# Performance work log

Hardware: AMD Instinct MI355X
Metric: run time of the kernel (lower is better)

The kernel has to match this reference:

```python
import jax, jax.numpy as jnp
import numpy as np

T = 16777216            # flat replay-buffer length (timesteps)
DISCOUNT = 0.99         # gamma
FINAL_REWARD = 0.0      # bootstrap value for the last timestep
TERM_PROB = 0.001       # ~1000-step episodes


def setup_inputs() -> dict:
    key = jax.random.key(0)
    k1, k2 = jax.random.split(key)
    reward = jax.random.normal(k1, (T,), dtype=jnp.float32)
    terminal = jax.random.bernoulli(k2, TERM_PROB, (T,))
    return {"terminal": terminal, "reward": reward}


def _discounted_cumret(terminal, reward):
    # Reverse-time linear recurrence (same math as tf.scan over reversed seq):
    #   c_t = r_t                      if terminal_t
    #   c_t = r_t + discount * c_{t+1} otherwise
    # i.e. c_t = a_t * c_{t+1} + b_t with a_t = discount*(1-term_t), b_t = r_t.
    # Expressed as a (log-depth) associative scan over the reversed sequence.
    a = jnp.where(terminal, jnp.zeros((), reward.dtype),
                  jnp.asarray(DISCOUNT, reward.dtype))
    a_rev = a[::-1]
    b_rev = reward[::-1]
    # fold the initializer (final_reward) into the first reversed element
    b_rev = b_rev.at[0].add(a_rev[0] * jnp.asarray(FINAL_REWARD, reward.dtype))

    def combine(e1, e2):
        # composition of affine maps x -> a*x + b (e1 applied first)
        a1, b1 = e1
        a2, b2 = e2
        return a1 * a2, a2 * b1 + b2

    _, y_rev = jax.lax.associative_scan(combine, (a_rev, b_rev))
    return y_rev[::-1]


def reference(terminal, reward):
    return _discounted_cumret(terminal, reward)
```

## Files before the change

kernel.cpp:

```cpp
#include <hip/hip_runtime.h>


constexpr int   TPB  = 256;
constexpr int   IPT  = 4;
constexpr int   TILE = TPB * IPT;
constexpr float DISC = 0.99f;

__device__ __forceinline__ void wave_suffix_scan(float& A, float& B, int lane) {
    #pragma unroll
    for (int off = 1; off < 64; off <<= 1) {
        float oA = __shfl_down(A, off, 64);
        float oB = __shfl_down(B, off, 64);
        if (lane + off < 64) { B = A * oB + B; A = A * oA; }
    }
}

__global__ __launch_bounds__(TPB) void k_agg(const int* __restrict__ term,
                                             const float* __restrict__ rew,
                                             float2* __restrict__ agg,
                                             long long T) {
    __shared__ float2 sW[TPB / 64];
    const int t = threadIdx.x;
    const int lane = t & 63, wav = t >> 6;
    const long long base = (long long)blockIdx.x * TILE + (long long)t * IPT;

    float r[IPT], a[IPT];
    if (base + IPT <= T) {
        float4 rv = *(const float4*)(rew + base);
        int4   tv = *(const int4*)(term + base);
        r[0]=rv.x; r[1]=rv.y; r[2]=rv.z; r[3]=rv.w;
        a[0]=tv.x?0.f:DISC; a[1]=tv.y?0.f:DISC; a[2]=tv.z?0.f:DISC; a[3]=tv.w?0.f:DISC;
    } else {
        #pragma unroll
        for (int k = 0; k < IPT; ++k) {
            long long i = base + k;
            if (i < T) { r[k]=rew[i]; a[k]=term[i]?0.f:DISC; }
            else       { r[k]=0.f;   a[k]=1.f; }
        }
    }

    float A = 1.f, B = 0.f;
    #pragma unroll
    for (int k = IPT - 1; k >= 0; --k) { B = a[k]*B + r[k]; A = a[k]*A; }

    wave_suffix_scan(A, B, lane);
    if (lane == 0) sW[wav] = make_float2(A, B);
    __syncthreads();
    if (t == 0) {
        float2 g = sW[0];
        #pragma unroll
        for (int w = 1; w < TPB / 64; ++w) {
            float2 h = sW[w];
            g.y = g.x * h.y + g.y; g.x = g.x * h.x;
        }
        agg[blockIdx.x] = g;
    }
}

__global__ __launch_bounds__(TPB) void k_mid(const float2* __restrict__ agg,
                                             float* __restrict__ yin,
                                             int numTiles) {
    __shared__ float2 sW[TPB / 64];
    const int t = threadIdx.x;
    const int lane = t & 63, wav = t >> 6;
    const int cpt = (numTiles + TPB - 1) / TPB;
    const int lo = t * cpt;

    float A = 1.f, B = 0.f;
    for (int k = cpt - 1; k >= 0; --k) {
        int g = lo + k;
        if (g < numTiles) {
            float2 v = agg[g];
            B = v.x * B + v.y; A = v.x * A;
        }
    }

    float IA = A, IB = B;
    wave_suffix_scan(IA, IB, lane);
    if (lane == 0) sW[wav] = make_float2(IA, IB);
    __syncthreads();

    float EWA = 1.f, EWB = 0.f;
    #pragma unroll
    for (int w = 0; w < TPB / 64; ++w)
        if (w > wav) { float2 h = sW[w]; EWB = EWA*h.y + EWB; EWA = EWA*h.x; }

    float EA = __shfl_down(IA, 1, 64);
    float EB = __shfl_down(IB, 1, 64);
    if (lane == 63) { EA = 1.f; EB = 0.f; }

    float x1 = EWB;
    float v  = EA * x1 + EB;
    for (int k = cpt - 1; k >= 0; --k) {
        int g = lo + k;
        if (g < numTiles) {
            yin[g] = v;
            float2 q = agg[g];
            v = q.x * v + q.y;
        }
    }
}

__global__ __launch_bounds__(TPB) void k_apply(const int* __restrict__ term,
                                               const float* __restrict__ rew,
                                               const float* __restrict__ yin,
                                               float* __restrict__ out,
                                               long long T) {
    __shared__ float2 sW[TPB / 64];
    const int t = threadIdx.x;
    const int lane = t & 63, wav = t >> 6;
    const long long base = (long long)blockIdx.x * TILE + (long long)t * IPT;

    float r[IPT], a[IPT];
    const bool fast = (base + IPT <= T);
    if (fast) {
        float4 rv = *(const float4*)(rew + base);
        int4   tv = *(const int4*)(term + base);
        r[0]=rv.x; r[1]=rv.y; r[2]=rv.z; r[3]=rv.w;
        a[0]=tv.x?0.f:DISC; a[1]=tv.y?0.f:DISC; a[2]=tv.z?0.f:DISC; a[3]=tv.w?0.f:DISC;
    } else {
        #pragma unroll
        for (int k = 0; k < IPT; ++k) {
            long long i = base + k;
            if (i < T) { r[k]=rew[i]; a[k]=term[i]?0.f:DISC; }
            else       { r[k]=0.f;   a[k]=1.f; }
        }
    }

    float A = 1.f, B = 0.f;
    #pragma unroll
    for (int k = IPT - 1; k >= 0; --k) { B = a[k]*B + r[k]; A = a[k]*A; }

    float IA = A, IB = B;
    wave_suffix_scan(IA, IB, lane);
    if (lane == 0) sW[wav] = make_float2(IA, IB);
    __syncthreads();

    float EWA = 1.f, EWB = 0.f;
    #pragma unroll
    for (int w = 0; w < TPB / 64; ++w)
        if (w > wav) { float2 h = sW[w]; EWB = EWA*h.y + EWB; EWA = EWA*h.x; }

    float EA = __shfl_down(IA, 1, 64);
    float EB = __shfl_down(IB, 1, 64);
    if (lane == 63) { EA = 1.f; EB = 0.f; }

    const float yt = yin[blockIdx.x];
    float x1 = EWA * yt + EWB;
    float y  = EA * x1 + EB;

    float yv[IPT];
    #pragma unroll
    for (int k = IPT - 1; k >= 0; --k) { y = a[k]*y + r[k]; yv[k] = y; }

    if (fast) {
        *(float4*)(out + base) = make_float4(yv[0], yv[1], yv[2], yv[3]);
    } else {
        #pragma unroll
        for (int k = 0; k < IPT; ++k) {
            long long i = base + k;
            if (i < T) out[i] = yv[k];
        }
    }
}

extern "C" void kernel_launch(void* const* d_in, const int* in_sizes, int n_in,
                              void* d_out, int out_size, void* d_ws, size_t ws_size,
                              hipStream_t stream) {
    const int*   term = (const int*)d_in[0];
    const float* rew  = (const float*)d_in[1];
    float*       out  = (float*)d_out;

    const long long T = (long long)in_sizes[1];
    const int numTiles = (int)((T + TILE - 1) / TILE);

    float2* agg = (float2*)d_ws;
    float*  yin = (float*)(agg + numTiles);

    k_agg  <<<numTiles, TPB, 0, stream>>>(term, rew, agg, T);
    k_mid  <<<1,        TPB, 0, stream>>>(agg, yin, numTiles);
    k_apply<<<numTiles, TPB, 0, stream>>>(term, rew, yin, out, T);
}
```

Before: 215.5 us.

## Replace reduce-then-scan with local scan plus sparse carry fix-up

The three-kernel reduce/mid/apply scan becomes two kernels. The first computes each block's local suffix scan and writes the output directly, along with the block aggregate and the index of the last terminal in the block. The second kernel has each block recompute the carry-in from all later block aggregates, then add carry*gamma^d only to the elements after the block's last terminal, so the inputs are read only once. Tiles grow to 32 items per thread, the terminal flags are packed into a bitmask, and the correction uses exp2f, which can differ slightly in rounding from sequential multiplication.

```diff
diff --git a/kernel.cpp b/kernel.cpp
--- a/kernel.cpp
+++ b/kernel.cpp
@@ -2,9 +2,10 @@
 
 
 constexpr int   TPB  = 256;
-constexpr int   IPT  = 4;
+constexpr int   IPT  = 32;
 constexpr int   TILE = TPB * IPT;
 constexpr float DISC = 0.99f;
+constexpr float L2DISC = -0.0144995696f;
 
 __device__ __forceinline__ void wave_suffix_scan(float& A, float& B, int lane) {
     #pragma unroll
@@ -15,152 +16,147 @@
     }
 }
 
-__global__ __launch_bounds__(TPB) void k_agg(const int* __restrict__ term,
-                                             const float* __restrict__ rew,
-                                             float2* __restrict__ agg,
-                                             long long T) {
-    __shared__ float2 sW[TPB / 64];
+__global__ __launch_bounds__(TPB) void k_local(
+        const int* __restrict__ term, const float* __restrict__ rew,
+        float* __restrict__ out, float2* __restrict__ agg,
+        int* __restrict__ lastT, long long T) {
+    __shared__ float2 sWA[TPB / 64];
+    __shared__ int    sLast[TPB / 64];
+
     const int t = threadIdx.x;
     const int lane = t & 63, wav = t >> 6;
-    const long long base = (long long)blockIdx.x * TILE + (long long)t * IPT;
+    const int b = blockIdx.x;
+    const long long lo   = (long long)b * TILE;
+    const long long base = lo + (long long)t * IPT;
+    const bool fast = (base + IPT <= T);
 
-    float r[IPT], a[IPT];
-    if (base + IPT <= T) {
-        float4 rv = *(const float4*)(rew + base);
-        int4   tv = *(const int4*)(term + base);
-        r[0]=rv.x; r[1]=rv.y; r[2]=rv.z; r[3]=rv.w;
-        a[0]=tv.x?0.f:DISC; a[1]=tv.y?0.f:DISC; a[2]=tv.z?0.f:DISC; a[3]=tv.w?0.f:DISC;
+    float r[IPT];
+    unsigned mask = 0;
+    if (fast) {
+        const float4* rp = (const float4*)(rew + base);
+        const int4*   tp = (const int4*)(term + base);
+        #pragma unroll
+        for (int q = 0; q < IPT / 4; ++q) {
+            float4 rv = rp[q];
+            int4   tv = tp[q];
+            r[4*q+0] = rv.x; r[4*q+1] = rv.y; r[4*q+2] = rv.z; r[4*q+3] = rv.w;
+            mask |= (tv.x ? 1u : 0u) << (4*q+0);
+            mask |= (tv.y ? 1u : 0u) << (4*q+1);
+            mask |= (tv.z ? 1u : 0u) << (4*q+2);
+            mask |= (tv.w ? 1u : 0u) << (4*q+3);
+        }
     } else {
         #pragma unroll
         for (int k = 0; k < IPT; ++k) {
             long long i = base + k;
-            if (i < T) { r[k]=rew[i]; a[k]=term[i]?0.f:DISC; }
-            else       { r[k]=0.f;   a[k]=1.f; }
+            if (i < T) { r[k] = rew[i]; mask |= (term[i] ? 1u : 0u) << k; }
+            else       { r[k] = 0.f; }
         }
     }
 
     float A = 1.f, B = 0.f;
     #pragma unroll
-    for (int k = IPT - 1; k >= 0; --k) { B = a[k]*B + r[k]; A = a[k]*A; }
-
-    wave_suffix_scan(A, B, lane);
-    if (lane == 0) sW[wav] = make_float2(A, B);
-    __syncthreads();
-    if (t == 0) {
-        float2 g = sW[0];
-        #pragma unroll
-        for (int w = 1; w < TPB / 64; ++w) {
-            float2 h = sW[w];
-            g.y = g.x * h.y + g.y; g.x = g.x * h.x;
-        }
-        agg[blockIdx.x] = g;
-    }
-}
-
-__global__ __launch_bounds__(TPB) void k_mid(const float2* __restrict__ agg,
-                                             float* __restrict__ yin,
-                                             int numTiles) {
-    __shared__ float2 sW[TPB / 64];
-    const int t = threadIdx.x;
-    const int lane = t & 63, wav = t >> 6;
-    const int cpt = (numTiles + TPB - 1) / TPB;
-    const int lo = t * cpt;
-
-    float A = 1.f, B = 0.f;
-    for (int k = cpt - 1; k >= 0; --k) {
-        int g = lo + k;
-        if (g < numTiles) {
-            float2 v = agg[g];
-            B = v.x * B + v.y; A = v.x * A;
-        }
+    for (int k = IPT - 1; k >= 0; --k) {
+        float ak = ((mask >> k) & 1u) ? 0.f : DISC;
+        if (!fast && base + k >= T) ak = 1.f;
+        B = ak * B + r[k]; A = ak * A;
     }
 
     float IA = A, IB = B;
     wave_suffix_scan(IA, IB, lane);
-    if (lane == 0) sW[wav] = make_float2(IA, IB);
+
+    int myLast = mask ? (int)(base + (31 - __clz(mask))) : -1;
+    #pragma unroll
+    for (int off = 32; off > 0; off >>= 1)
+        myLast = max(myLast, __shfl_down(myLast, off, 64));
+
+    if (lane == 0) { sWA[wav] = make_float2(IA, IB); sLast[wav] = myLast; }
     __syncthreads();
+
+    if (t == 0) {
+        float2 g = sWA[0];
+        int lt = sLast[0];
+        #pragma unroll
+        for (int w = 1; w < TPB / 64; ++w) {
+            float2 h = sWA[w];
+            g.y = g.x * h.y + g.y; g.x = g.x * h.x;
+            lt = max(lt, sLast[w]);
+        }
+        agg[b] = g;
+        lastT[b] = max(lt, (int)lo - 1);
+    }
 
     float EWA = 1.f, EWB = 0.f;
     #pragma unroll
     for (int w = 0; w < TPB / 64; ++w)
-        if (w > wav) { float2 h = sW[w]; EWB = EWA*h.y + EWB; EWA = EWA*h.x; }
+        if (w > wav) { float2 h = sWA[w]; EWB = EWA*h.y + EWB; EWA = EWA*h.x; }
 
     float EA = __shfl_down(IA, 1, 64);
     float EB = __shfl_down(IB, 1, 64);
     if (lane == 63) { EA = 1.f; EB = 0.f; }
 
-    float x1 = EWB;
-    float v  = EA * x1 + EB;
-    for (int k = cpt - 1; k >= 0; --k) {
-        int g = lo + k;
-        if (g < numTiles) {
-            yin[g] = v;
-            float2 q = agg[g];
-            v = q.x * v + q.y;
+    float y = EA * EWB + EB;
+
+    #pragma unroll
+    for (int k = IPT - 1; k >= 0; --k) {
+        float ak = ((mask >> k) & 1u) ? 0.f : DISC;
+        if (!fast && base + k >= T) ak = 1.f;
+        y = ak * y + r[k]; r[k] = y;
+    }
+
+    if (fast) {
+        float4* op = (float4*)(out + base);
+        #pragma unroll
+        for (int q = 0; q < IPT / 4; ++q)
+            op[q] = make_float4(r[4*q+0], r[4*q+1], r[4*q+2], r[4*q+3]);
+    } else {
+        #pragma unroll
+        for (int k = 0; k < IPT; ++k) {
+            long long i = base + k;
+            if (i < T) out[i] = r[k];
         }
     }
 }
 
-__global__ __launch_bounds__(TPB) void k_apply(const int* __restrict__ term,
-                                               const float* __restrict__ rew,
-                                               const float* __restrict__ yin,
-                                               float* __restrict__ out,
-                                               long long T) {
-    __shared__ float2 sW[TPB / 64];
+__global__ __launch_bounds__(TPB) void k_fix(
+        const float2* __restrict__ agg, const int* __restrict__ lastT,
+        float* __restrict__ out, int numBlocks, long long T) {
+    __shared__ float2 sWB[TPB / 64];
+
     const int t = threadIdx.x;
     const int lane = t & 63, wav = t >> 6;
-    const long long base = (long long)blockIdx.x * TILE + (long long)t * IPT;
+    const int b = blockIdx.x;
 
-    float r[IPT], a[IPT];
-    const bool fast = (base + IPT <= T);
-    if (fast) {
-        float4 rv = *(const float4*)(rew + base);
-        int4   tv = *(const int4*)(term + base);
-        r[0]=rv.x; r[1]=rv.y; r[2]=rv.z; r[3]=rv.w;
-        a[0]=tv.x?0.f:DISC; a[1]=tv.y?0.f:DISC; a[2]=tv.z?0.f:DISC; a[3]=tv.w?0.f:DISC;
-    } else {
-        #pragma unroll
-        for (int k = 0; k < IPT; ++k) {
-            long long i = base + k;
-            if (i < T) { r[k]=rew[i]; a[k]=term[i]?0.f:DISC; }
-            else       { r[k]=0.f;   a[k]=1.f; }
+    const int cpt = (numBlocks + TPB - 1) / TPB;
+    float VA = 1.f, VB = 0.f;
+    #pragma unroll
+    for (int k = cpt - 1; k >= 0; --k) {
+        int g = t * cpt + k;
+        if (g > b && g < numBlocks) {
+            float2 q = agg[g];
+            VB = q.x * VB + q.y; VA = q.x * VA;
         }
     }
-
-    float A = 1.f, B = 0.f;
-    #pragma unroll
-    for (int k = IPT - 1; k >= 0; --k) { B = a[k]*B + r[k]; A = a[k]*A; }
-
-    float IA = A, IB = B;
-    wave_suffix_scan(IA, IB, lane);
-    if (lane == 0) sW[wav] = make_float2(IA, IB);
+    wave_suffix_scan(VA, VB, lane);
+    if (lane == 0) sWB[wav] = make_float2(VA, VB);
     __syncthreads();
 
-    float EWA = 1.f, EWB = 0.f;
+    float FA = sWB[0].x, FB = sWB[0].y;
     #pragma unroll
-    for (int w = 0; w < TPB / 64; ++w)
-        if (w > wav) { float2 h = sW[w]; EWB = EWA*h.y + EWB; EWA = EWA*h.x; }
+    for (int w = 1; w < TPB / 64; ++w) {
+        float2 h = sWB[w];
+        FB = FA * h.y + FB; FA = FA * h.x;
+    }
+    const float yin = FB;
+    if (yin == 0.f) return;
 
-    float EA = __shfl_down(IA, 1, 64);
-    float EB = __shfl_down(IB, 1, 64);
-    if (lane == 63) { EA = 1.f; EB = 0.f; }
+    const long long lo = (long long)b * TILE;
+    const long long hi = min(lo + TILE, T) - 1;
+    const long long start = (long long)lastT[b] + 1;
 
-    const float yt = yin[blockIdx.x];
-    float x1 = EWA * yt + EWB;
-    float y  = EA * x1 + EB;
-
-    float yv[IPT];
-    #pragma unroll
-    for (int k = IPT - 1; k >= 0; --k) { y = a[k]*y + r[k]; yv[k] = y; }
-
-    if (fast) {
-        *(float4*)(out + base) = make_float4(yv[0], yv[1], yv[2], yv[3]);
-    } else {
-        #pragma unroll
-        for (int k = 0; k < IPT; ++k) {
-            long long i = base + k;
-            if (i < T) out[i] = yv[k];
-        }
+    for (long long i = start + t; i <= hi; i += TPB) {
+        float d = (float)(int)(hi + 1 - i);
+        out[i] += exp2f(d * L2DISC) * yin;
     }
 }
 
@@ -172,12 +168,11 @@
     float*       out  = (float*)d_out;
 
     const long long T = (long long)in_sizes[1];
-    const int numTiles = (int)((T + TILE - 1) / TILE);
+    const int numBlocks = (int)((T + TILE - 1) / TILE);
 
-    float2* agg = (float2*)d_ws;
-    float*  yin = (float*)(agg + numTiles);
+    float2* agg   = (float2*)d_ws;
+    int*    lastT = (int*)(agg + numBlocks);
 
-    k_agg  <<<numTiles, TPB, 0, stream>>>(term, rew, agg, T);
-    k_mid  <<<1,        TPB, 0, stream>>>(agg, yin, numTiles);
-    k_apply<<<numTiles, TPB, 0, stream>>>(term, rew, yin, out, T);
+    k_local<<<numBlocks, TPB, 0, stream>>>(term, rew, out, agg, lastT, T);
+    k_fix  <<<numBlocks, TPB, 0, stream>>>(agg, lastT, out, numBlocks, T);
 }
```

Measured after the change: 183.3 us. -15.0%, faster.
